# Kernel tuning notes

Measured on AMD Instinct MI355X. Metric: run time of the kernel, lower is better.

The kernel has to match this reference:

```python
import jax, jax.numpy as jnp
import numpy as np

HEADS = 16
EMBED = 1024
D_K = EMBED // HEADS


def setup_inputs() -> dict:
    key = jax.random.key(0)
    ks = jax.random.split(key, 11)
    B, S, E = 4, 2048, EMBED
    sc = 0.02
    return {
        "query": jax.random.normal(ks[0], (B, S, E), jnp.float32),
        "key_": jax.random.normal(ks[1], (B, S, E), jnp.float32),
        "value": jax.random.normal(ks[2], (B, S, E), jnp.float32),
        "Wq": jax.random.normal(ks[3], (E, E), jnp.float32) * sc,
        "bq": jnp.zeros((E,), jnp.float32),
        "Wk": jax.random.normal(ks[4], (E, E), jnp.float32) * sc,
        "bk": jnp.zeros((E,), jnp.float32),
        "Wv": jax.random.normal(ks[5], (E, E), jnp.float32) * sc,
        "bv": jnp.zeros((E,), jnp.float32),
        "Wo": jax.random.normal(ks[6], (E, D_K), jnp.float32) * sc,  # out: Linear(heads*d_k -> d_k)
        "bo": jnp.zeros((D_K,), jnp.float32),
    }


def reference(query, key_, value, Wq, bq, Wk, bk, Wv, bv, Wo, bo):
    B, S, E = query.shape
    H, Dk = HEADS, D_K
    # QKV projections
    q = query @ Wq + bq          # (B,S,E)
    k = key_ @ Wk + bk
    v = value @ Wv + bv
    # split heads -> (B,H,S,Dk)
    q = q.reshape(B, S, H, Dk).transpose(0, 2, 1, 3)
    k = k.reshape(B, S, H, Dk).transpose(0, 2, 1, 3)
    v = v.reshape(B, S, H, Dk).transpose(0, 2, 1, 3)
    # attention: softmax(QK^T / sqrt(d_k)) V
    scores = jnp.einsum("bhqd,bhkd->bhqk", q, k) / jnp.sqrt(jnp.asarray(Dk, q.dtype))
    attn = jax.nn.softmax(scores, axis=-1)
    ctx = jnp.einsum("bhqk,bhkd->bhqd", attn, v)
    ctx = ctx.transpose(0, 2, 1, 3).reshape(B, S, E)
    # output projection (E -> d_k, as in source)
    return ctx @ Wo + bo
```

## Files before the change

kernel.cpp:

```cpp
#include <hip/hip_runtime.h>
#include <hip/hip_bf16.h>
#include <cstdint>
#include <cstddef>

#define DEVI static __device__ __forceinline__

typedef unsigned short u16;
typedef unsigned int u32;
typedef __bf16 bf16_t;
typedef __bf16 bf16x8 __attribute__((ext_vector_type(8)));
typedef float f32x4 __attribute__((ext_vector_type(4)));
typedef float f32x16 __attribute__((ext_vector_type(16)));

union U16x8 { uint4 u; bf16x8 v; };
union PU { uint2 u2[2]; bf16x8 v; };

#define QSCALE 0.1803368801111204f

DEVI void gload_lds16(const void* g, void* l) {
  __builtin_amdgcn_global_load_lds((const __attribute__((address_space(1))) void*)g,
                                   (__attribute__((address_space(3))) void*)l, 16, 0, 0);
}
DEVI void wait_vmcnt0() { asm volatile("s_waitcnt vmcnt(0)" ::: "memory"); }

DEVI u32 pack2(float a, float b) {
  u16 x = __builtin_bit_cast(u16, (bf16_t)a);
  u16 y = __builtin_bit_cast(u16, (bf16_t)b);
  return (u32)x | ((u32)y << 16);
}

DEVI u32 cvt_pk_bf16(float lo, float hi) {
  u32 r;
  asm("v_cvt_pk_bf16_f32 %0, %1, %2" : "=v"(r) : "v"(lo), "v"(hi));
  return r;
}

DEVI f32x16 mfma32(bf16x8 a, bf16x8 b, f32x16 c) {
  return __builtin_amdgcn_mfma_f32_32x32x16_bf16(a, b, c, 0, 0, 0);
}

DEVI bf16x8 lds_frag(const char* base, int row, int koff, int swz) {
  U16x8 u;
  u.u = *(const uint4*)(base + row * 128 + (koff ^ swz));
  return u.v;
}

__global__ __launch_bounds__(256) void k_cvt3(
    const float* __restrict__ a, const float* __restrict__ b, const float* __restrict__ c,
    bf16_t* __restrict__ dst) {
  int which = blockIdx.x >> 10;
  int bb = blockIdx.x & 1023;
  const float* s = which == 0 ? a : which == 1 ? b : c;
  u16* d = (u16*)dst + (size_t)which * 8192 * 1024;
  size_t base = ((size_t)bb * 256 + threadIdx.x) * 8;
  #pragma unroll
  for (int p = 0; p < 4; ++p) {
    size_t i = base + (size_t)p * 2097152;
    float4 f0 = *(const float4*)(s + i);
    float4 f1 = *(const float4*)(s + i + 4);
    uint4 o;
    o.x = pack2(f0.x, f0.y); o.y = pack2(f0.z, f0.w);
    o.z = pack2(f1.x, f1.y); o.w = pack2(f1.z, f1.w);
    *(uint4*)(d + i) = o;
  }
}

__global__ __launch_bounds__(256) void k_transpose_convert(
    const float* __restrict__ src, bf16_t* __restrict__ dst, int R, int C, float scale) {
  int tiles_c = C >> 6;
  int tc = blockIdx.x % tiles_c;
  int tr = blockIdx.x / tiles_c;
  int r0 = tr << 6, c0 = tc << 6;
  __shared__ u16 tile[64][65];
  int t = threadIdx.x;
  #pragma unroll
  for (int p = 0; p < 4; ++p) {
    int idx = t + p * 256;
    int i = idx >> 4, j4 = (idx & 15) * 4;
    float4 f = *(const float4*)(src + (size_t)(r0 + i) * C + c0 + j4);
    tile[i][j4 + 0] = __builtin_bit_cast(u16, (bf16_t)(f.x * scale));
    tile[i][j4 + 1] = __builtin_bit_cast(u16, (bf16_t)(f.y * scale));
    tile[i][j4 + 2] = __builtin_bit_cast(u16, (bf16_t)(f.z * scale));
    tile[i][j4 + 3] = __builtin_bit_cast(u16, (bf16_t)(f.w * scale));
  }
  __syncthreads();
  #pragma unroll
  for (int p = 0; p < 2; ++p) {
    int idx = t + p * 256;
    int j = idx >> 3, i0 = (idx & 7) * 8;
    u16 us[8];
    #pragma unroll
    for (int e = 0; e < 8; ++e) us[e] = tile[i0 + e][j];
    uint4 o;
    o.x = (u32)us[0] | ((u32)us[1] << 16);
    o.y = (u32)us[2] | ((u32)us[3] << 16);
    o.z = (u32)us[4] | ((u32)us[5] << 16);
    o.w = (u32)us[6] | ((u32)us[7] << 16);
    *(uint4*)((u16*)dst + (size_t)(c0 + j) * R + r0 + i0) = o;
  }
}

template<bool PRE>
__global__ __launch_bounds__(256) void k_proj_gemm(
    const float* __restrict__ Aq, const float* __restrict__ Ak, const float* __restrict__ Av,
    const bf16_t* __restrict__ Abf,
    const bf16_t* __restrict__ WqT, const bf16_t* __restrict__ WkT, const bf16_t* __restrict__ WvT,
    const float* __restrict__ bq, const float* __restrict__ bk, const float* __restrict__ bv,
    bf16_t* __restrict__ qh, bf16_t* __restrict__ kh, bf16_t* __restrict__ vh) {
  int bx = blockIdx.x;
  int which = bx >> 9;
  int tt = bx & 511;
  int tile_m = tt & 63;
  int tile_n = tt >> 6;
  const float* A    = which == 0 ? Aq : which == 1 ? Ak : Av;
  const bf16_t* Ab  = Abf + (size_t)which * 8192 * 1024;
  const bf16_t* WT  = which == 0 ? WqT : which == 1 ? WkT : WvT;
  const float* bias = which == 0 ? bq : which == 1 ? bk : bv;
  const float bscale = which == 0 ? QSCALE : 1.0f;
  bf16_t* dst       = which == 0 ? qh : which == 1 ? kh : vh;

  const int t = threadIdx.x;
  const int l = t & 63;
  const int w = t >> 6;
  const int wm = w >> 1, wn = w & 1;
  const int c = l & 15, g = l >> 4;
  const int row0 = tile_m << 7;
  const int n0 = tile_n << 7;

  __shared__ __align__(16) char As[128 * 64 * 2];
  __shared__ __align__(16) char Bs[128 * 64 * 2];

  f32x4 acc[4][4];
  #pragma unroll
  for (int i = 0; i < 4; ++i)
    #pragma unroll
    for (int j = 0; j < 4; ++j) acc[i][j] = (f32x4){0.f, 0.f, 0.f, 0.f};

  const int arow = t >> 1, ahalf = t & 1;
  const float* abase = A + (size_t)(row0 + arow) * 1024 + ahalf * 32;

  for (int kt = 0; kt < 16; ++kt) {
    __syncthreads();
    if constexpr (PRE) {
      #pragma unroll
      for (int cc = 0; cc < 4; ++cc) {
        int slot = w * 256 + cc * 64 + l;
        int row = slot >> 3, chs = slot & 7;
        const bf16_t* src = Ab + (size_t)(row0 + row) * 1024 + kt * 64 + ((chs ^ (row & 7)) << 3);
        gload_lds16(src, As + (w * 256 + cc * 64) * 16);
      }
    } else {
      const float* ap = abase + kt * 64;
      float4 f[8];
      #pragma unroll
      for (int i = 0; i < 8; ++i) f[i] = *(const float4*)(ap + i * 4);
      #pragma unroll
      for (int wch = 0; wch < 4; ++wch) {
        int chunk = ahalf * 4 + wch;
        int chs = chunk ^ (arow & 7);
        uint4 o;
        o.x = pack2(f[wch * 2].x, f[wch * 2].y);
        o.y = pack2(f[wch * 2].z, f[wch * 2].w);
        o.z = pack2(f[wch * 2 + 1].x, f[wch * 2 + 1].y);
        o.w = pack2(f[wch * 2 + 1].z, f[wch * 2 + 1].w);
        *(uint4*)(As + arow * 128 + chs * 16) = o;
      }
    }
    #pragma unroll
    for (int cc = 0; cc < 4; ++cc) {
      int slot = w * 256 + cc * 64 + l;
      int row = slot >> 3, chs = slot & 7;
      const bf16_t* src = WT + (size_t)(n0 + row) * 1024 + kt * 64 + ((chs ^ (row & 7)) << 3);
      gload_lds16(src, Bs + (w * 256 + cc * 64) * 16);
    }
    wait_vmcnt0();
    __syncthreads();
    #pragma unroll
    for (int kk = 0; kk < 2; ++kk) {
      bf16x8 af[4], bfr[4];
      #pragma unroll
      for (int mi = 0; mi < 4; ++mi) {
        int row = wm * 64 + mi * 16 + c;
        U16x8 u; u.u = *(const uint4*)(As + row * 128 + ((kk * 64 + g * 16) ^ ((c & 7) << 4)));
        af[mi] = u.v;
      }
      #pragma unroll
      for (int ni = 0; ni < 4; ++ni) {
        int row = wn * 64 + ni * 16 + c;
        U16x8 u; u.u = *(const uint4*)(Bs + row * 128 + ((kk * 64 + g * 16) ^ ((c & 7) << 4)));
        bfr[ni] = u.v;
      }
      #pragma unroll
      for (int mi = 0; mi < 4; ++mi)
        #pragma unroll
        for (int ni = 0; ni < 4; ++ni)
          acc[mi][ni] = __builtin_amdgcn_mfma_f32_16x16x32_bf16(af[mi], bfr[ni], acc[mi][ni], 0, 0, 0);
    }
  }
  u16* dd = (u16*)dst;
  #pragma unroll
  for (int ni = 0; ni < 4; ++ni) {
    int col = n0 + wn * 64 + ni * 16 + c;
    float bb = bias[col] * bscale;
    int h = col >> 6, d = col & 63;
    #pragma unroll
    for (int mi = 0; mi < 4; ++mi) {
      #pragma unroll
      for (int r = 0; r < 4; ++r) {
        int rowg = row0 + wm * 64 + mi * 16 + g * 4 + r;
        int b = rowg >> 11, s = rowg & 2047;
        float vv = acc[mi][ni][r] + bb;
        size_t idx = (((size_t)b * 16 + h) * 2048 + s) * 64 + d;
        dd[idx] = __builtin_bit_cast(u16, (bf16_t)vv);
      }
    }
  }
}

__global__ __launch_bounds__(256) void k_transpose_v(
    const bf16_t* __restrict__ vh, bf16_t* __restrict__ vT) {
  int bh = blockIdx.x >> 5, st = blockIdx.x & 31;
  int s0 = st << 6;
  __shared__ __align__(16) u16 tile[64][72];
  int t = threadIdx.x;
  const u16* src = (const u16*)vh + ((size_t)bh * 2048 + s0) * 64;
  #pragma unroll
  for (int p = 0; p < 2; ++p) {
    int idx = t + p * 256;
    int s = idx >> 3, d0 = (idx & 7) * 8;
    uint4 v = *(const uint4*)(src + s * 64 + d0);
    *(uint4*)(&tile[s][d0]) = v;
  }
  __syncthreads();
  u16* dst = (u16*)vT + (size_t)bh * 64 * 2048 + s0;
  #pragma unroll
  for (int p = 0; p < 2; ++p) {
    int idx = t + p * 256;
    int d = idx >> 3, s1 = (idx & 7) * 8;
    u16 us[8];
    #pragma unroll
    for (int e = 0; e < 8; ++e) us[e] = tile[s1 + e][d];
    uint4 o;
    o.x = (u32)us[0] | ((u32)us[1] << 16);
    o.y = (u32)us[2] | ((u32)us[3] << 16);
    o.z = (u32)us[4] | ((u32)us[5] << 16);
    o.w = (u32)us[6] | ((u32)us[7] << 16);
    *(uint4*)(dst + (size_t)d * 2048 + s1) = o;
  }
}

__global__ __launch_bounds__(256, 4) void k_attn(
    const bf16_t* __restrict__ qh, const bf16_t* __restrict__ kh,
    const bf16_t* __restrict__ vT, bf16_t* __restrict__ ctx) {
  const int bid = blockIdx.x;
  const int bx = ((bid & 7) << 7) | (bid >> 3);
  const int bh = bx >> 4;
  const int qt = bx & 15;
  const int q0 = qt << 7;
  const int t = threadIdx.x, l = t & 63, w = t >> 6;
  const int q = l & 31;
  const int hi = l >> 5;
  const int swz = (q & 7) << 4;

  __shared__ __align__(16) char Ks[64 * 128];
  __shared__ __align__(16) char Vs[64 * 128];
  __shared__ __align__(16) char Ps[4][32 * 136];
  __shared__ __align__(16) float Dn[4][32];
  char* Pb = Ps[w];

  const u16* qrow = (const u16*)qh + ((size_t)bh * 2048 + q0 + w * 32 + q) * 64;
  bf16x8 qf0, qf1, qf2, qf3;
  {
    U16x8 u;
    u.u = *(const uint4*)(qrow + 0 * 16 + hi * 8); qf0 = u.v;
    u.u = *(const uint4*)(qrow + 1 * 16 + hi * 8); qf1 = u.v;
    u.u = *(const uint4*)(qrow + 2 * 16 + hi * 8); qf2 = u.v;
    u.u = *(const uint4*)(qrow + 3 * 16 + hi * 8); qf3 = u.v;
  }

  const f32x16 z16 = {0.f,0.f,0.f,0.f, 0.f,0.f,0.f,0.f, 0.f,0.f,0.f,0.f, 0.f,0.f,0.f,0.f};
  f32x16 oc0 = z16, oc1 = z16;
  float l_run = 0.f;

  const u16* kbh = (const u16*)kh + (size_t)bh * 2048 * 64;
  const u16* vbh = (const u16*)vT + (size_t)bh * 64 * 2048;

  for (int kv = 0; kv < 32; ++kv) {
    const int kbase = kv << 6;
    #pragma unroll
    for (int cc = 0; cc < 2; ++cc) {
      int slot = w * 128 + cc * 64 + l;
      int row = slot >> 3, chs = slot & 7;
      gload_lds16(kbh + (size_t)(kbase + row) * 64 + ((chs ^ (row & 7)) << 3),
                  Ks + (w * 128 + cc * 64) * 16);
      gload_lds16(vbh + (size_t)row * 2048 + kbase + ((chs ^ (row & 7)) << 3),
                  Vs + (w * 128 + cc * 64) * 16);
    }
    wait_vmcnt0();
    __syncthreads();

    float lt = 0.f;
    #pragma unroll
    for (int tt = 0; tt < 2; ++tt) {
      const int arow = tt * 32 + q;
      f32x16 st = z16;
      __builtin_amdgcn_s_setprio(1);
      st = mfma32(lds_frag(Ks, arow, 0 * 32 + hi * 16, swz), qf0, st);
      st = mfma32(lds_frag(Ks, arow, 1 * 32 + hi * 16, swz), qf1, st);
      st = mfma32(lds_frag(Ks, arow, 2 * 32 + hi * 16, swz), qf2, st);
      st = mfma32(lds_frag(Ks, arow, 3 * 32 + hi * 16, swz), qf3, st);
      __builtin_amdgcn_s_setprio(0);
      #pragma unroll
      for (int qd = 0; qd < 4; ++qd) {
        float e0 = __builtin_amdgcn_exp2f(st[qd * 4 + 0]);
        float e1 = __builtin_amdgcn_exp2f(st[qd * 4 + 1]);
        float e2 = __builtin_amdgcn_exp2f(st[qd * 4 + 2]);
        float e3 = __builtin_amdgcn_exp2f(st[qd * 4 + 3]);
        lt += (e0 + e1) + (e2 + e3);
        uint2 pw;
        pw.x = cvt_pk_bf16(e0, e1);
        pw.y = cvt_pk_bf16(e2, e3);
        *(uint2*)(Pb + q * 136 + tt * 64 + qd * 16 + hi * 8) = pw;
      }
    }
    l_run += lt;

    __builtin_amdgcn_s_setprio(1);
    #pragma unroll
    for (int ks = 0; ks < 4; ++ks) {
      PU pu;
      pu.u2[0] = *(const uint2*)(Pb + q * 136 + ks * 32 + hi * 16);
      pu.u2[1] = *(const uint2*)(Pb + q * 136 + ks * 32 + hi * 16 + 8);
      oc0 = mfma32(pu.v, lds_frag(Vs, q,      ks * 32 + hi * 16, swz), oc0);
      oc1 = mfma32(pu.v, lds_frag(Vs, 32 + q, ks * 32 + hi * 16, swz), oc1);
    }
    __builtin_amdgcn_s_setprio(0);
    __syncthreads();
  }

  l_run += __shfl_xor(l_run, 32);
  Dn[w][q] = 1.f / l_run;
  __syncthreads();

  const int b = bh >> 4, hh = bh & 15;
  u16* cb = (u16*)ctx;
  #pragma unroll
  for (int qd = 0; qd < 4; ++qd) {
    float4 dv = *(const float4*)&Dn[w][qd * 8 + hi * 4];
    #pragma unroll
    for (int r = 0; r < 4; ++r) {
      float inv = (&dv.x)[r];
      int qrow_g = q0 + w * 32 + qd * 8 + hi * 4 + r;
      size_t base = ((size_t)b * 2048 + qrow_g) * 1024 + hh * 64;
      float v0 = oc0[qd * 4 + r] * inv;
      float v1 = oc1[qd * 4 + r] * inv;
      cb[base + q]      = __builtin_bit_cast(u16, (bf16_t)v0);
      cb[base + 32 + q] = __builtin_bit_cast(u16, (bf16_t)v1);
    }
  }
}

__global__ __launch_bounds__(256) void k_out_gemm(
    const bf16_t* __restrict__ ctx, const bf16_t* __restrict__ WoT,
    const float* __restrict__ bo, float* __restrict__ out) {
  int tile_m = blockIdx.x;
  const int t = threadIdx.x, l = t & 63, w = t >> 6;
  const int wm = w >> 1, wn = w & 1;
  const int c = l & 15, g = l >> 4;
  const int row0 = tile_m << 7;

  __shared__ __align__(16) char As[128 * 64 * 2];
  __shared__ __align__(16) char Bs[64 * 64 * 2];

  f32x4 acc[4][2];
  #pragma unroll
  for (int i = 0; i < 4; ++i)
    #pragma unroll
    for (int j = 0; j < 2; ++j) acc[i][j] = (f32x4){0.f, 0.f, 0.f, 0.f};

  for (int kt = 0; kt < 16; ++kt) {
    __syncthreads();
    #pragma unroll
    for (int cc = 0; cc < 4; ++cc) {
      int slot = w * 256 + cc * 64 + l;
      int row = slot >> 3, chs = slot & 7;
      const bf16_t* src = ctx + (size_t)(row0 + row) * 1024 + kt * 64 + ((chs ^ (row & 7)) << 3);
      gload_lds16(src, As + (w * 256 + cc * 64) * 16);
    }
    #pragma unroll
    for (int cc = 0; cc < 2; ++cc) {
      int slot = w * 128 + cc * 64 + l;
      int row = slot >> 3, chs = slot & 7;
      const bf16_t* src = WoT + (size_t)row * 1024 + kt * 64 + ((chs ^ (row & 7)) << 3);
      gload_lds16(src, Bs + (w * 128 + cc * 64) * 16);
    }
    wait_vmcnt0();
    __syncthreads();
    #pragma unroll
    for (int kk = 0; kk < 2; ++kk) {
      bf16x8 af[4], bfr[2];
      #pragma unroll
      for (int mi = 0; mi < 4; ++mi) {
        int row = wm * 64 + mi * 16 + c;
        U16x8 u; u.u = *(const uint4*)(As + row * 128 + ((kk * 64 + g * 16) ^ ((c & 7) << 4)));
        af[mi] = u.v;
      }
      #pragma unroll
      for (int ni = 0; ni < 2; ++ni) {
        int row = wn * 32 + ni * 16 + c;
        U16x8 u; u.u = *(const uint4*)(Bs + row * 128 + ((kk * 64 + g * 16) ^ ((c & 7) << 4)));
        bfr[ni] = u.v;
      }
      #pragma unroll
      for (int mi = 0; mi < 4; ++mi)
        #pragma unroll
        for (int ni = 0; ni < 2; ++ni)
          acc[mi][ni] = __builtin_amdgcn_mfma_f32_16x16x32_bf16(af[mi], bfr[ni], acc[mi][ni], 0, 0, 0);
    }
  }
  #pragma unroll
  for (int ni = 0; ni < 2; ++ni) {
    int col = wn * 32 + ni * 16 + c;
    float bb = bo[col];
    #pragma unroll
    for (int mi = 0; mi < 4; ++mi) {
      #pragma unroll
      for (int r = 0; r < 4; ++r) {
        int rowg = row0 + wm * 64 + mi * 16 + g * 4 + r;
        out[(size_t)rowg * 64 + col] = acc[mi][ni][r] + bb;
      }
    }
  }
}

extern "C" void kernel_launch(void* const* d_in, const int* in_sizes, int n_in,
                              void* d_out, int out_size, void* d_ws, size_t ws_size,
                              hipStream_t stream) {
  (void)in_sizes; (void)n_in; (void)out_size;
  const float* query = (const float*)d_in[0];
  const float* key_  = (const float*)d_in[1];
  const float* value = (const float*)d_in[2];
  const float* Wq = (const float*)d_in[3];
  const float* bq = (const float*)d_in[4];
  const float* Wk = (const float*)d_in[5];
  const float* bk = (const float*)d_in[6];
  const float* Wv = (const float*)d_in[7];
  const float* bv = (const float*)d_in[8];
  const float* Wo = (const float*)d_in[9];
  const float* bo = (const float*)d_in[10];
  float* out = (float*)d_out;

  char* ws = (char*)d_ws;
  bf16_t* WqT = (bf16_t*)(ws + (size_t)0);
  bf16_t* WkT = (bf16_t*)(ws + ((size_t)2 << 20));
  bf16_t* WvT = (bf16_t*)(ws + ((size_t)4 << 20));
  bf16_t* WoT = (bf16_t*)(ws + ((size_t)6 << 20));
  bf16_t* qhd = (bf16_t*)(ws + ((size_t)8 << 20));
  bf16_t* khd = (bf16_t*)(ws + ((size_t)24 << 20));
  bf16_t* vhd = (bf16_t*)(ws + ((size_t)40 << 20));
  bf16_t* vT  = (bf16_t*)(ws + ((size_t)56 << 20));
  bf16_t* ctx = (bf16_t*)(ws + ((size_t)72 << 20));
  bf16_t* Abf = (bf16_t*)(ws + ((size_t)88 << 20));

  const bool pre = ws_size >= ((size_t)137 << 20);

  k_transpose_convert<<<256, 256, 0, stream>>>(Wq, WqT, 1024, 1024, QSCALE);
  k_transpose_convert<<<256, 256, 0, stream>>>(Wk, WkT, 1024, 1024, 1.0f);
  k_transpose_convert<<<256, 256, 0, stream>>>(Wv, WvT, 1024, 1024, 1.0f);
  k_transpose_convert<<<16, 256, 0, stream>>>(Wo, WoT, 1024, 64, 1.0f);

  if (pre) {
    k_cvt3<<<3072, 256, 0, stream>>>(query, key_, value, Abf);
    k_proj_gemm<true><<<1536, 256, 0, stream>>>(query, key_, value, Abf, WqT, WkT, WvT,
                                                bq, bk, bv, qhd, khd, vhd);
  } else {
    k_proj_gemm<false><<<1536, 256, 0, stream>>>(query, key_, value, Abf, WqT, WkT, WvT,
                                                 bq, bk, bv, qhd, khd, vhd);
  }
  k_transpose_v<<<2048, 256, 0, stream>>>(vhd, vT);
  k_attn<<<1024, 256, 0, stream>>>(qhd, khd, vT, ctx);
  k_out_gemm<<<64, 256, 0, stream>>>(ctx, WoT, bo, out);
}
```

Before: 205.4 us.

## Double-buffer K/V in attention, keep P in registers via permlane swaps, drop pre-convert

Attention now double-buffers K/V tiles in LDS, issuing the next tile's loads before computing on the current one. The softmax probabilities are repacked into MFMA A-operand layout with v_permlane32_swap instead of a round-trip through LDS, which also removes that LDS buffer. The separate fp32-to-bf16 pre-conversion kernel is removed, so the projection GEMM always converts inline using cvt_pk_bf16. Doubling the K/V buffers raises LDS use, and dropping the pre-convert path may slow the projection stage.

```diff
diff --git a/kernel.cpp b/kernel.cpp
--- a/kernel.cpp
+++ b/kernel.cpp
@@ -13,7 +13,7 @@
 typedef float f32x16 __attribute__((ext_vector_type(16)));
 
 union U16x8 { uint4 u; bf16x8 v; };
-union PU { uint2 u2[2]; bf16x8 v; };
+union PU { u32 w[4]; bf16x8 v; };
 
 #define QSCALE 0.1803368801111204f
 
@@ -35,6 +35,10 @@
   return r;
 }
 
+DEVI void permswap(u32& a, u32& b) {
+  asm("v_permlane32_swap_b32 %0, %1" : "+v"(a), "+v"(b));
+}
+
 DEVI f32x16 mfma32(bf16x8 a, bf16x8 b, f32x16 c) {
   return __builtin_amdgcn_mfma_f32_32x32x16_bf16(a, b, c, 0, 0, 0);
 }
@@ -43,26 +47,6 @@
   U16x8 u;
   u.u = *(const uint4*)(base + row * 128 + (koff ^ swz));
   return u.v;
-}
-
-__global__ __launch_bounds__(256) void k_cvt3(
-    const float* __restrict__ a, const float* __restrict__ b, const float* __restrict__ c,
-    bf16_t* __restrict__ dst) {
-  int which = blockIdx.x >> 10;
-  int bb = blockIdx.x & 1023;
-  const float* s = which == 0 ? a : which == 1 ? b : c;
-  u16* d = (u16*)dst + (size_t)which * 8192 * 1024;
-  size_t base = ((size_t)bb * 256 + threadIdx.x) * 8;
-  #pragma unroll
-  for (int p = 0; p < 4; ++p) {
-    size_t i = base + (size_t)p * 2097152;
-    float4 f0 = *(const float4*)(s + i);
-    float4 f1 = *(const float4*)(s + i + 4);
-    uint4 o;
-    o.x = pack2(f0.x, f0.y); o.y = pack2(f0.z, f0.w);
-    o.z = pack2(f1.x, f1.y); o.w = pack2(f1.z, f1.w);
-    *(uint4*)(d + i) = o;
-  }
 }
 
 __global__ __launch_bounds__(256) void k_transpose_convert(
@@ -100,10 +84,8 @@
   }
 }
 
-template<bool PRE>
 __global__ __launch_bounds__(256) void k_proj_gemm(
     const float* __restrict__ Aq, const float* __restrict__ Ak, const float* __restrict__ Av,
-    const bf16_t* __restrict__ Abf,
     const bf16_t* __restrict__ WqT, const bf16_t* __restrict__ WkT, const bf16_t* __restrict__ WvT,
     const float* __restrict__ bq, const float* __restrict__ bk, const float* __restrict__ bv,
     bf16_t* __restrict__ qh, bf16_t* __restrict__ kh, bf16_t* __restrict__ vh) {
@@ -113,7 +95,6 @@
   int tile_m = tt & 63;
   int tile_n = tt >> 6;
   const float* A    = which == 0 ? Aq : which == 1 ? Ak : Av;
-  const bf16_t* Ab  = Abf + (size_t)which * 8192 * 1024;
   const bf16_t* WT  = which == 0 ? WqT : which == 1 ? WkT : WvT;
   const float* bias = which == 0 ? bq : which == 1 ? bk : bv;
   const float bscale = which == 0 ? QSCALE : 1.0f;
@@ -141,15 +122,7 @@
 
   for (int kt = 0; kt < 16; ++kt) {
     __syncthreads();
-    if constexpr (PRE) {
-      #pragma unroll
-      for (int cc = 0; cc < 4; ++cc) {
-        int slot = w * 256 + cc * 64 + l;
-        int row = slot >> 3, chs = slot & 7;
-        const bf16_t* src = Ab + (size_t)(row0 + row) * 1024 + kt * 64 + ((chs ^ (row & 7)) << 3);
-        gload_lds16(src, As + (w * 256 + cc * 64) * 16);
-      }
-    } else {
+    {
       const float* ap = abase + kt * 64;
       float4 f[8];
       #pragma unroll
@@ -159,10 +132,10 @@
         int chunk = ahalf * 4 + wch;
         int chs = chunk ^ (arow & 7);
         uint4 o;
-        o.x = pack2(f[wch * 2].x, f[wch * 2].y);
-        o.y = pack2(f[wch * 2].z, f[wch * 2].w);
-        o.z = pack2(f[wch * 2 + 1].x, f[wch * 2 + 1].y);
-        o.w = pack2(f[wch * 2 + 1].z, f[wch * 2 + 1].w);
+        o.x = cvt_pk_bf16(f[wch * 2].x, f[wch * 2].y);
+        o.y = cvt_pk_bf16(f[wch * 2].z, f[wch * 2].w);
+        o.z = cvt_pk_bf16(f[wch * 2 + 1].x, f[wch * 2 + 1].y);
+        o.w = cvt_pk_bf16(f[wch * 2 + 1].z, f[wch * 2 + 1].w);
         *(uint4*)(As + arow * 128 + chs * 16) = o;
       }
     }
@@ -262,11 +235,9 @@
   const int hi = l >> 5;
   const int swz = (q & 7) << 4;
 
-  __shared__ __align__(16) char Ks[64 * 128];
-  __shared__ __align__(16) char Vs[64 * 128];
-  __shared__ __align__(16) char Ps[4][32 * 136];
+  __shared__ __align__(16) char Ks[2][64 * 128];
+  __shared__ __align__(16) char Vs[2][64 * 128];
   __shared__ __align__(16) float Dn[4][32];
-  char* Pb = Ps[w];
 
   const u16* qrow = (const u16*)qh + ((size_t)bh * 2048 + q0 + w * 32 + q) * 64;
   bf16x8 qf0, qf1, qf2, qf3;
@@ -285,56 +256,65 @@
   const u16* kbh = (const u16*)kh + (size_t)bh * 2048 * 64;
   const u16* vbh = (const u16*)vT + (size_t)bh * 64 * 2048;
 
-  for (int kv = 0; kv < 32; ++kv) {
-    const int kbase = kv << 6;
+  auto stage = [&](int kvi, int buf) {
+    int kbase = kvi << 6;
     #pragma unroll
     for (int cc = 0; cc < 2; ++cc) {
       int slot = w * 128 + cc * 64 + l;
       int row = slot >> 3, chs = slot & 7;
       gload_lds16(kbh + (size_t)(kbase + row) * 64 + ((chs ^ (row & 7)) << 3),
-                  Ks + (w * 128 + cc * 64) * 16);
+                  Ks[buf] + (w * 128 + cc * 64) * 16);
       gload_lds16(vbh + (size_t)row * 2048 + kbase + ((chs ^ (row & 7)) << 3),
-                  Vs + (w * 128 + cc * 64) * 16);
-    }
-    wait_vmcnt0();
-    __syncthreads();
-
-    float lt = 0.f;
+                  Vs[buf] + (w * 128 + cc * 64) * 16);
+    }
+  };
+
+  stage(0, 0);
+  wait_vmcnt0();
+  __syncthreads();
+
+  for (int kv = 0; kv < 32; ++kv) {
+    const int cur = kv & 1;
+    if (kv < 31) stage(kv + 1, cur ^ 1);
+    const char* Kc = Ks[cur];
+    const char* Vc = Vs[cur];
+
     #pragma unroll
     for (int tt = 0; tt < 2; ++tt) {
       const int arow = tt * 32 + q;
       f32x16 st = z16;
       __builtin_amdgcn_s_setprio(1);
-      st = mfma32(lds_frag(Ks, arow, 0 * 32 + hi * 16, swz), qf0, st);
-      st = mfma32(lds_frag(Ks, arow, 1 * 32 + hi * 16, swz), qf1, st);
-      st = mfma32(lds_frag(Ks, arow, 2 * 32 + hi * 16, swz), qf2, st);
-      st = mfma32(lds_frag(Ks, arow, 3 * 32 + hi * 16, swz), qf3, st);
+      st = mfma32(lds_frag(Kc, arow, 0 * 32 + hi * 16, swz), qf0, st);
+      st = mfma32(lds_frag(Kc, arow, 1 * 32 + hi * 16, swz), qf1, st);
+      st = mfma32(lds_frag(Kc, arow, 2 * 32 + hi * 16, swz), qf2, st);
+      st = mfma32(lds_frag(Kc, arow, 3 * 32 + hi * 16, swz), qf3, st);
       __builtin_amdgcn_s_setprio(0);
-      #pragma unroll
-      for (int qd = 0; qd < 4; ++qd) {
-        float e0 = __builtin_amdgcn_exp2f(st[qd * 4 + 0]);
-        float e1 = __builtin_amdgcn_exp2f(st[qd * 4 + 1]);
-        float e2 = __builtin_amdgcn_exp2f(st[qd * 4 + 2]);
-        float e3 = __builtin_amdgcn_exp2f(st[qd * 4 + 3]);
-        lt += (e0 + e1) + (e2 + e3);
-        uint2 pw;
-        pw.x = cvt_pk_bf16(e0, e1);
-        pw.y = cvt_pk_bf16(e2, e3);
-        *(uint2*)(Pb + q * 136 + tt * 64 + qd * 16 + hi * 8) = pw;
-      }
-    }
-    l_run += lt;
-
-    __builtin_amdgcn_s_setprio(1);
-    #pragma unroll
-    for (int ks = 0; ks < 4; ++ks) {
-      PU pu;
-      pu.u2[0] = *(const uint2*)(Pb + q * 136 + ks * 32 + hi * 16);
-      pu.u2[1] = *(const uint2*)(Pb + q * 136 + ks * 32 + hi * 16 + 8);
-      oc0 = mfma32(pu.v, lds_frag(Vs, q,      ks * 32 + hi * 16, swz), oc0);
-      oc1 = mfma32(pu.v, lds_frag(Vs, 32 + q, ks * 32 + hi * 16, swz), oc1);
-    }
-    __builtin_amdgcn_s_setprio(0);
+
+      float e[16];
+      #pragma unroll
+      for (int i = 0; i < 16; ++i) {
+        e[i] = __builtin_amdgcn_exp2f(st[i]);
+        l_run += e[i];
+      }
+
+      #pragma unroll
+      for (int cc = 0; cc < 2; ++cc) {
+        u32 a  = cvt_pk_bf16(e[8 * cc + 0], e[8 * cc + 1]);
+        u32 b  = cvt_pk_bf16(e[8 * cc + 4], e[8 * cc + 5]);
+        u32 c2 = cvt_pk_bf16(e[8 * cc + 2], e[8 * cc + 3]);
+        u32 d  = cvt_pk_bf16(e[8 * cc + 6], e[8 * cc + 7]);
+        permswap(a, b);
+        permswap(c2, d);
+        PU pu;
+        pu.w[0] = a; pu.w[1] = c2; pu.w[2] = b; pu.w[3] = d;
+        const int ks = tt * 2 + cc;
+        __builtin_amdgcn_s_setprio(1);
+        oc0 = mfma32(pu.v, lds_frag(Vc, q,      ks * 32 + hi * 16, swz), oc0);
+        oc1 = mfma32(pu.v, lds_frag(Vc, 32 + q, ks * 32 + hi * 16, swz), oc1);
+        __builtin_amdgcn_s_setprio(0);
+      }
+    }
+    wait_vmcnt0();
     __syncthreads();
   }
 
@@ -436,7 +416,7 @@
 extern "C" void kernel_launch(void* const* d_in, const int* in_sizes, int n_in,
                               void* d_out, int out_size, void* d_ws, size_t ws_size,
                               hipStream_t stream) {
-  (void)in_sizes; (void)n_in; (void)out_size;
+  (void)in_sizes; (void)n_in; (void)out_size; (void)ws_size;
   const float* query = (const float*)d_in[0];
   const float* key_  = (const float*)d_in[1];
   const float* value = (const float*)d_in[2];
@@ -460,23 +440,14 @@
   bf16_t* vhd = (bf16_t*)(ws + ((size_t)40 << 20));
   bf16_t* vT  = (bf16_t*)(ws + ((size_t)56 << 20));
   bf16_t* ctx = (bf16_t*)(ws + ((size_t)72 << 20));
-  bf16_t* Abf = (bf16_t*)(ws + ((size_t)88 << 20));
-
-  const bool pre = ws_size >= ((size_t)137 << 20);
 
   k_transpose_convert<<<256, 256, 0, stream>>>(Wq, WqT, 1024, 1024, QSCALE);
   k_transpose_convert<<<256, 256, 0, stream>>>(Wk, WkT, 1024, 1024, 1.0f);
   k_transpose_convert<<<256, 256, 0, stream>>>(Wv, WvT, 1024, 1024, 1.0f);
   k_transpose_convert<<<16, 256, 0, stream>>>(Wo, WoT, 1024, 64, 1.0f);
 
-  if (pre) {
-    k_cvt3<<<3072, 256, 0, stream>>>(query, key_, value, Abf);
-    k_proj_gemm<true><<<1536, 256, 0, stream>>>(query, key_, value, Abf, WqT, WkT, WvT,
-                                                bq, bk, bv, qhd, khd, vhd);
-  } else {
-    k_proj_gemm<false><<<1536, 256, 0, stream>>>(query, key_, value, Abf, WqT, WkT, WvT,
-                                                 bq, bk, bv, qhd, khd, vhd);
-  }
+  k_proj_gemm<<<1536, 256, 0, stream>>>(query, key_, value, WqT, WkT, WvT,
+                                        bq, bk, bv, qhd, khd, vhd);
   k_transpose_v<<<2048, 256, 0, stream>>>(vhd, vT);
   k_attn<<<1024, 256, 0, stream>>>(qhd, khd, vT, ctx);
   k_out_gemm<<<64, 256, 0, stream>>>(ctx, WoT, bo, out);
```

After: 233.0 us. +13.4%, slower.
